# Kernel optimization log

Measured on AMD Instinct MI355X. Metric: run time of the kernel, lower is better.

The kernel has to match this reference:

```python
import jax, jax.numpy as jnp
import numpy as np

N = 1048576   # points per render chunk (16384 rays x 64 samples)
W = 64        # MLP width
IN = 32       # n_features_per_level * n_levels
LD = 36
HC = 15       # num_hidcolordim


def _linear_params(key, fan_in, fan_out):
    kw, kb = jax.random.split(key)
    bound = 1.0 / np.sqrt(fan_in)
    Wm = jax.random.uniform(kw, (fan_in, fan_out), jnp.float32, -bound, bound)
    b = jax.random.uniform(kb, (fan_out,), jnp.float32, -bound, bound)
    return Wm, b


def setup_inputs() -> dict:
    key = jax.random.key(0)
    ks = jax.random.split(key, 10)
    emb_points = jax.random.normal(ks[0], (N, IN), jnp.float32)
    enc_dir = jax.random.normal(ks[1], (N, LD + 3), jnp.float32)
    W_in, b_in = _linear_params(ks[2], IN, W)          # MLPinput
    W0, b0 = _linear_params(ks[3], W, W)               # MLPmid0 (num_hiddense=1)
    Wd, bd = _linear_params(ks[4], W, 1 + HC)          # Denseout
    Wc, bc = _linear_params(ks[5], HC + LD + 3, W)     # colorlayerin
    W1a, b1a = _linear_params(ks[6], W, W)             # MLPmid1 layer 0
    W1b, b1b = _linear_params(ks[7], W, W)             # MLPmid1 layer 1
    Wo, bo = _linear_params(ks[8], W, 3)               # colorout
    return dict(emb_points=emb_points, enc_dir=enc_dir,
                W_in=W_in, b_in=b_in, W0=W0, b0=b0, Wd=Wd, bd=bd,
                Wc=Wc, bc=bc, W1a=W1a, b1a=b1a, W1b=W1b, b1b=b1b,
                Wo=Wo, bo=bo)


def reference(emb_points, enc_dir, W_in, b_in, W0, b0, Wd, bd,
              Wc, bc, W1a, b1a, W1b, b1b, Wo, bo):
    relu = jax.nn.relu
    x = relu(emb_points @ W_in + b_in)          # [N, 64]
    x = relu(x @ W0 + b0)                       # MLPmid0
    x = x @ Wd + bd                             # [N, 16]
    dense = x[..., :1]                          # density, no activation
    h = x[..., 1:]                              # [N, 15]
    h = relu(jnp.concatenate([h, enc_dir], axis=-1) @ Wc + bc)  # [N, 64]
    h = relu(h @ W1a + b1a)                     # MLPmid1
    h = relu(h @ W1b + b1b)
    color = h @ Wo + bo                         # [N, 3]
    return jnp.concatenate([color, dense], axis=-1)  # [N, 4]
```

## Files before the change

### kernel.cpp

```cpp
#include <hip/hip_runtime.h>


#define WAVES_PER_BLOCK 8
#define BLOCK 512
#define GRID 512
#define XSTR 72
#define NFRAG 40

typedef _Float16 half8 __attribute__((ext_vector_type(8)));
typedef _Float16 half4 __attribute__((ext_vector_type(4)));
typedef _Float16 half2v __attribute__((ext_vector_type(2)));
typedef float float4v __attribute__((ext_vector_type(4)));
typedef float float4u __attribute__((ext_vector_type(4), aligned(4)));

__device__ __forceinline__ half8 wfrag(const float* W, int ld, int row0, int col, int nrow) {
  half8 r;
#pragma unroll
  for (int j = 0; j < 8; ++j) {
    int rr = row0 + j;
    float v = (rr < nrow) ? W[(size_t)rr * ld + col] : 0.f;
    r[j] = (_Float16)v;
  }
  return r;
}

__device__ half8 make_frag(int f, int q, int c,
                           const float* Win, const float* W0m, const float* Wd,
                           const float* Wc, const float* W1a, const float* W1b,
                           const float* Wo) {
  if (f < 4) return wfrag(Win, 64, 8 * q, 16 * f + c, 32);
  if (f < 12) { int t = (f - 4) >> 1, ks = (f - 4) & 1;
    return wfrag(W0m, 64, 32 * ks + 8 * q, 16 * t + c, 64); }
  if (f < 14) { int ks = f - 12;
    return wfrag(Wd, 16, 32 * ks + 8 * q, c, 64); }
  if (f < 22) { int t = (f - 14) >> 1, ks = (f - 14) & 1;
    half8 r;
#pragma unroll
    for (int j = 0; j < 8; ++j) {
      int k = 32 * ks + 8 * q + j;
      float v;
      if (k < 39) v = Wc[(size_t)(15 + k) * 64 + 16 * t + c];
      else if (k < 54) v = Wc[(size_t)(k - 39) * 64 + 16 * t + c];
      else v = 0.f;
      r[j] = (_Float16)v;
    }
    return r; }
  if (f < 30) { int t = (f - 22) >> 1, ks = (f - 22) & 1;
    return wfrag(W1a, 64, 32 * ks + 8 * q, 16 * t + c, 64); }
  if (f < 38) { int t = (f - 30) >> 1, ks = (f - 30) & 1;
    return wfrag(W1b, 64, 32 * ks + 8 * q, 16 * t + c, 64); }
  { int ks = f - 38;
    half8 r;
#pragma unroll
    for (int j = 0; j < 8; ++j) {
      float v = (c < 3) ? Wo[(size_t)(32 * ks + 8 * q + j) * 3 + c] : 0.f;
      r[j] = (_Float16)v;
    }
    return r; }
}

__global__ __launch_bounds__(BLOCK, 4) void nerf_fused(
    const float* __restrict__ emb, const float* __restrict__ enc,
    const float* __restrict__ Win, const float* __restrict__ bin,
    const float* __restrict__ W0m, const float* __restrict__ b0v,
    const float* __restrict__ Wd, const float* __restrict__ bd,
    const float* __restrict__ Wc, const float* __restrict__ bc,
    const float* __restrict__ W1a, const float* __restrict__ b1a,
    const float* __restrict__ W1b, const float* __restrict__ b1b,
    const float* __restrict__ Wo, const float* __restrict__ bo,
    float* __restrict__ out, int npts)
{
  __shared__ __align__(16) _Float16 s_w[NFRAG * 512];
  __shared__ __align__(16) float s_bias[352];
  __shared__ __align__(16) _Float16 s_X[WAVES_PER_BLOCK][32 * XSTR];

  const int tid = threadIdx.x;
  const int wib = tid >> 6;
  const int lane = tid & 63;
  const int q = lane >> 4;
  const int c = lane & 15;

  for (int i = tid; i < 352; i += BLOCK) {
    float v;
    if (i < 64) v = bin[i];
    else if (i < 128) v = b0v[i - 64];
    else if (i < 144) v = bd[i - 128];
    else if (i < 208) v = bc[i - 144];
    else if (i < 272) v = b1a[i - 208];
    else if (i < 336) v = b1b[i - 272];
    else v = (i - 336 < 3) ? bo[i - 336] : 0.f;
    s_bias[i] = v;
  }

  for (int f = wib * 5; f < wib * 5 + 5; ++f) {
    half8 r = make_frag(f, q, c, Win, W0m, Wd, Wc, W1a, W1b, Wo);
    *(half8*)&s_w[f * 512 + lane * 8] = r;
  }

  __syncthreads();

  _Float16* Xw = &s_X[wib][0];
#define OSTP(p) ((float*)(Xw + (p) * XSTR + 64))

  const int totalWaves = gridDim.x * WAVES_PER_BLOCK;
  const int waveId = blockIdx.x * WAVES_PER_BLOCK + wib;
  const int ntiles = npts >> 5;

  int tile = waveId;
  if (tile >= ntiles) return;

#define RW(f) (*(const half8*)&s_w[(f) * 512 + lane * 8])

  float4v e0[2], e1[2];
  float4u na0[2], na1[2], nb[2];
#pragma unroll
  for (int g = 0; g < 2; ++g) { na0[g] = (float4u){0,0,0,0}; na1[g] = (float4u){0,0,0,0}; nb[g] = (float4u){0,0,0,0}; }
  {
#pragma unroll
    for (int g = 0; g < 2; ++g) {
      const float* ep = emb + (size_t)(tile * 32 + 16 * g + c) * 32 + 8 * q;
      e0[g] = *(const float4v*)ep;
      e1[g] = *(const float4v*)(ep + 4);
      const float* np = enc + (size_t)(tile * 32 + 16 * g + c) * 39;
      na0[g] = *(const float4u*)(np + 8 * q);
      na1[g] = *(const float4u*)(np + 8 * q + 4);
      if (q == 0) nb[g] = *(const float4u*)(np + 32);
      else if (q == 1) { nb[g][0] = np[36]; nb[g][1] = np[37]; }
      else if (q == 2) nb[g][0] = np[38];
    }
  }

  const float4v z4 = {0.f, 0.f, 0.f, 0.f};
  float4v acc[4][2];
  half8 x[2][2];

#define READX() do { \
    _Pragma("unroll") for (int g = 0; g < 2; ++g) { \
      x[g][0] = *(const half8*)&Xw[(16 * g + c) * XSTR + 8 * q]; \
      x[g][1] = *(const half8*)&Xw[(16 * g + c) * XSTR + 32 + 8 * q]; \
    } \
  } while (0)

#define LAYER64(FB, BOFF) do { \
    _Pragma("unroll") for (int t = 0; t < 4; ++t) { \
      half8 wa = RW((FB) + 2 * t), wb = RW((FB) + 2 * t + 1); \
      _Pragma("unroll") for (int g = 0; g < 2; ++g) { \
        acc[t][g] = __builtin_amdgcn_mfma_f32_16x16x32_f16(wa, x[g][0], z4, 0, 0, 0); \
        acc[t][g] = __builtin_amdgcn_mfma_f32_16x16x32_f16(wb, x[g][1], acc[t][g], 0, 0, 0); \
      } \
    } \
    _Pragma("unroll") for (int t = 0; t < 4; ++t) { \
      float4v bb = *(const float4v*)&s_bias[(BOFF) + 16 * t + 4 * q]; \
      _Pragma("unroll") for (int g = 0; g < 2; ++g) { \
        half4 h; \
        _Pragma("unroll") for (int r = 0; r < 4; ++r) \
          h[r] = (_Float16)fmaxf(acc[t][g][r] + bb[r], 0.f); \
        *(half4*)&Xw[(16 * g + c) * XSTR + 16 * t + 4 * q] = h; \
      } \
    } \
  } while (0)

  for (; tile < ntiles; tile += totalWaves) {
    const int nt0 = tile + totalWaves;
    const int nextTile = (nt0 < ntiles) ? nt0 : tile;

    half8 bf[2];
#pragma unroll
    for (int g = 0; g < 2; ++g)
#pragma unroll
      for (int j = 0; j < 4; ++j) { bf[g][j] = (_Float16)e0[g][j]; bf[g][4 + j] = (_Float16)e1[g][j]; }
    {
#pragma unroll
      for (int g = 0; g < 2; ++g) {
        const float* ep = emb + (size_t)(nextTile * 32 + 16 * g + c) * 32 + 8 * q;
        e0[g] = *(const float4v*)ep;
        e1[g] = *(const float4v*)(ep + 4);
      }
    }
#pragma unroll
    for (int t = 0; t < 4; ++t) {
      half8 wt = RW(t);
#pragma unroll
      for (int g = 0; g < 2; ++g)
        acc[t][g] = __builtin_amdgcn_mfma_f32_16x16x32_f16(wt, bf[g], z4, 0, 0, 0);
    }
#pragma unroll
    for (int t = 0; t < 4; ++t) {
      float4v bb = *(const float4v*)&s_bias[0 + 16 * t + 4 * q];
#pragma unroll
      for (int g = 0; g < 2; ++g) {
        half4 h;
#pragma unroll
        for (int r = 0; r < 4; ++r) h[r] = (_Float16)fmaxf(acc[t][g][r] + bb[r], 0.f);
        *(half4*)&Xw[(16 * g + c) * XSTR + 16 * t + 4 * q] = h;
      }
    }

    READX();
    LAYER64(4, 64);

    READX();
    float4v a3[2];
    {
      half8 wa = RW(12), wb = RW(13);
#pragma unroll
      for (int g = 0; g < 2; ++g) {
        a3[g] = __builtin_amdgcn_mfma_f32_16x16x32_f16(wa, x[g][0], z4, 0, 0, 0);
        a3[g] = __builtin_amdgcn_mfma_f32_16x16x32_f16(wb, x[g][1], a3[g], 0, 0, 0);
      }
    }

#pragma unroll
    for (int g = 0; g < 2; ++g) {
      _Float16* Xp = &Xw[(16 * g + c) * XSTR];
      half8 ha;
#pragma unroll
      for (int j = 0; j < 4; ++j) { ha[j] = (_Float16)na0[g][j]; ha[4 + j] = (_Float16)na1[g][j]; }
      *(half8*)&Xp[8 * q] = ha;
      if (q == 0) {
        half4 hb;
#pragma unroll
        for (int r = 0; r < 4; ++r) hb[r] = (_Float16)nb[g][r];
        *(half4*)&Xp[32] = hb;
      } else if (q == 1) {
        half2v hb; hb[0] = (_Float16)nb[g][0]; hb[1] = (_Float16)nb[g][1];
        *(half2v*)&Xp[36] = hb;
      } else if (q == 2) {
        Xp[38] = (_Float16)nb[g][0];
      } else {
        half2v zz2 = {(_Float16)0.f, (_Float16)0.f};
        *(half2v*)&Xp[54] = zz2;
        half8 zz8 = {};
        *(half8*)&Xp[56] = zz8;
      }
    }
    {
#pragma unroll
      for (int g = 0; g < 2; ++g) {
        const float* np = enc + (size_t)(nextTile * 32 + 16 * g + c) * 39;
        na0[g] = *(const float4u*)(np + 8 * q);
        na1[g] = *(const float4u*)(np + 8 * q + 4);
        if (q == 0) nb[g] = *(const float4u*)(np + 32);
        else if (q == 1) { nb[g][0] = np[36]; nb[g][1] = np[37]; }
        else if (q == 2) nb[g][0] = np[38];
      }
    }

    {
      float4v bb = *(const float4v*)&s_bias[128 + 4 * q];
#pragma unroll
      for (int g = 0; g < 2; ++g)
#pragma unroll
        for (int r = 0; r < 4; ++r) {
          float v = a3[g][r] + bb[r];
          int f = 4 * q + r;
          if (f == 0) OSTP(16 * g + c)[3] = v;
          else Xw[(16 * g + c) * XSTR + 38 + f] = (_Float16)v;
        }
    }

    READX();
    LAYER64(14, 144);

    READX();
    LAYER64(22, 208);
    READX();
    LAYER64(30, 272);

    READX();
    {
      half8 wa = RW(38), wb = RW(39);
      float4v bb = *(const float4v*)&s_bias[336 + 4 * q];
#pragma unroll
      for (int g = 0; g < 2; ++g) {
        float4v a7 = __builtin_amdgcn_mfma_f32_16x16x32_f16(wa, x[g][0], z4, 0, 0, 0);
        a7 = __builtin_amdgcn_mfma_f32_16x16x32_f16(wb, x[g][1], a7, 0, 0, 0);
        if (q == 0) {
          float* op = OSTP(16 * g + c);
          op[0] = a7[0] + bb[0];
          op[1] = a7[1] + bb[1];
          op[2] = a7[2] + bb[2];
        }
      }
    }

    out[(size_t)tile * 128 + lane]      = OSTP(lane >> 2)[lane & 3];
    out[(size_t)tile * 128 + 64 + lane] = OSTP(16 + (lane >> 2))[lane & 3];
  }
#undef READX
#undef LAYER64
#undef RW
#undef OSTP
}

extern "C" void kernel_launch(void* const* d_in, const int* in_sizes, int n_in,
                              void* d_out, int out_size, void* d_ws, size_t ws_size,
                              hipStream_t stream) {
  (void)d_ws; (void)ws_size; (void)out_size;
  if (n_in < 16) return;
  const float* emb = (const float*)d_in[0];
  const float* enc = (const float*)d_in[1];
  const float* Win = (const float*)d_in[2];
  const float* bin = (const float*)d_in[3];
  const float* W0m = (const float*)d_in[4];
  const float* b0v = (const float*)d_in[5];
  const float* Wd  = (const float*)d_in[6];
  const float* bd  = (const float*)d_in[7];
  const float* Wc  = (const float*)d_in[8];
  const float* bc  = (const float*)d_in[9];
  const float* W1a = (const float*)d_in[10];
  const float* b1a = (const float*)d_in[11];
  const float* W1b = (const float*)d_in[12];
  const float* b1b = (const float*)d_in[13];
  const float* Wo  = (const float*)d_in[14];
  const float* bo  = (const float*)d_in[15];
  float* out = (float*)d_out;
  const int npts = in_sizes[0] / 32;

  nerf_fused<<<GRID, BLOCK, 0, stream>>>(emb, enc, Win, bin, W0m, b0v, Wd, bd,
                                         Wc, bc, W1a, b1a, W1b, b1b, Wo, bo,
                                         out, npts);
}
```

Before: 355.0 us.

## Keep MLP activations in registers via permuted-K weight fragments, drop LDS staging

Permutes the K ordering of the packed weight fragments so that each MFMA output fragment (4 rows per lane) can be fed straight back as the B operand of the next layer. Activations therefore stay in registers instead of being written to and read back from a per-wave LDS buffer. The biases are folded into the MFMA accumulator init, and outputs are written directly as float4 per point. This removes LDS round-trips and the per-wave LDS allocation, which may raise occupancy, but it makes the Wc concat layout and its weight packing more intricate.

```diff
diff --git a/kernel.cpp b/kernel.cpp
--- a/kernel.cpp
+++ b/kernel.cpp
@@ -4,59 +4,85 @@
 #define WAVES_PER_BLOCK 8
 #define BLOCK 512
 #define GRID 512
-#define XSTR 72
 #define NFRAG 40
 
 typedef _Float16 half8 __attribute__((ext_vector_type(8)));
 typedef _Float16 half4 __attribute__((ext_vector_type(4)));
-typedef _Float16 half2v __attribute__((ext_vector_type(2)));
 typedef float float4v __attribute__((ext_vector_type(4)));
 typedef float float4u __attribute__((ext_vector_type(4), aligned(4)));
 
-__device__ __forceinline__ half8 wfrag(const float* W, int ld, int row0, int col, int nrow) {
-  half8 r;
-#pragma unroll
-  for (int j = 0; j < 8; ++j) {
-    int rr = row0 + j;
-    float v = (rr < nrow) ? W[(size_t)rr * ld + col] : 0.f;
-    r[j] = (_Float16)v;
-  }
-  return r;
+#define CAT8(a, b) __builtin_shufflevector((a), (b), 0, 1, 2, 3, 4, 5, 6, 7)
+
+__device__ __forceinline__ int permk(int u, int q, int j) {
+  return 32 * u + 16 * (j >> 2) + 4 * q + (j & 3);
 }
 
 __device__ half8 make_frag(int f, int q, int c,
                            const float* Win, const float* W0m, const float* Wd,
                            const float* Wc, const float* W1a, const float* W1b,
                            const float* Wo) {
-  if (f < 4) return wfrag(Win, 64, 8 * q, 16 * f + c, 32);
-  if (f < 12) { int t = (f - 4) >> 1, ks = (f - 4) & 1;
-    return wfrag(W0m, 64, 32 * ks + 8 * q, 16 * t + c, 64); }
-  if (f < 14) { int ks = f - 12;
-    return wfrag(Wd, 16, 32 * ks + 8 * q, c, 64); }
-  if (f < 22) { int t = (f - 14) >> 1, ks = (f - 14) & 1;
-    half8 r;
-#pragma unroll
-    for (int j = 0; j < 8; ++j) {
-      int k = 32 * ks + 8 * q + j;
-      float v;
-      if (k < 39) v = Wc[(size_t)(15 + k) * 64 + 16 * t + c];
-      else if (k < 54) v = Wc[(size_t)(k - 39) * 64 + 16 * t + c];
-      else v = 0.f;
-      r[j] = (_Float16)v;
-    }
-    return r; }
-  if (f < 30) { int t = (f - 22) >> 1, ks = (f - 22) & 1;
-    return wfrag(W1a, 64, 32 * ks + 8 * q, 16 * t + c, 64); }
-  if (f < 38) { int t = (f - 30) >> 1, ks = (f - 30) & 1;
-    return wfrag(W1b, 64, 32 * ks + 8 * q, 16 * t + c, 64); }
-  { int ks = f - 38;
-    half8 r;
-#pragma unroll
-    for (int j = 0; j < 8; ++j) {
-      float v = (c < 3) ? Wo[(size_t)(32 * ks + 8 * q + j) * 3 + c] : 0.f;
-      r[j] = (_Float16)v;
-    }
-    return r; }
+  half8 r;
+  if (f < 4) {
+#pragma unroll
+    for (int j = 0; j < 8; ++j)
+      r[j] = (_Float16)Win[(size_t)(8 * q + j) * 64 + 16 * f + c];
+    return r;
+  }
+  if (f < 12) {
+    int mb = (f - 4) >> 1, u = (f - 4) & 1;
+#pragma unroll
+    for (int j = 0; j < 8; ++j)
+      r[j] = (_Float16)W0m[(size_t)permk(u, q, j) * 64 + 16 * mb + c];
+    return r;
+  }
+  if (f < 14) {
+    int u = f - 12;
+#pragma unroll
+    for (int j = 0; j < 8; ++j)
+      r[j] = (_Float16)Wd[(size_t)permk(u, q, j) * 16 + c];
+    return r;
+  }
+  if (f < 22) {
+    int mb = (f - 14) >> 1, u = (f - 14) & 1;
+    if (u == 0) {
+#pragma unroll
+      for (int i = 0; i < 4; ++i) {
+        int hs = 4 * q + i;
+        r[i] = (hs == 0) ? (_Float16)0.f
+                         : (_Float16)Wc[(size_t)(hs - 1) * 64 + 16 * mb + c];
+        int e = 32 + 4 * q + i;
+        r[4 + i] = (e < 39) ? (_Float16)Wc[(size_t)(15 + e) * 64 + 16 * mb + c]
+                            : (_Float16)0.f;
+      }
+    } else {
+#pragma unroll
+      for (int j = 0; j < 8; ++j)
+        r[j] = (_Float16)Wc[(size_t)(15 + 8 * q + j) * 64 + 16 * mb + c];
+    }
+    return r;
+  }
+  if (f < 30) {
+    int mb = (f - 22) >> 1, u = (f - 22) & 1;
+#pragma unroll
+    for (int j = 0; j < 8; ++j)
+      r[j] = (_Float16)W1a[(size_t)permk(u, q, j) * 64 + 16 * mb + c];
+    return r;
+  }
+  if (f < 38) {
+    int mb = (f - 30) >> 1, u = (f - 30) & 1;
+#pragma unroll
+    for (int j = 0; j < 8; ++j)
+      r[j] = (_Float16)W1b[(size_t)permk(u, q, j) * 64 + 16 * mb + c];
+    return r;
+  }
+  {
+    int u = f - 38;
+#pragma unroll
+    for (int j = 0; j < 8; ++j)
+      r[j] = (c < 3) ? (_Float16)Wo[(size_t)permk(u, q, j) * 3 + c]
+                     : (_Float16)0.f;
+    return r;
+  }
 }
 
 __global__ __launch_bounds__(BLOCK, 4) void nerf_fused(
@@ -72,7 +98,6 @@
 {
   __shared__ __align__(16) _Float16 s_w[NFRAG * 512];
   __shared__ __align__(16) float s_bias[352];
-  __shared__ __align__(16) _Float16 s_X[WAVES_PER_BLOCK][32 * XSTR];
 
   const int tid = threadIdx.x;
   const int wib = tid >> 6;
@@ -99,9 +124,6 @@
 
   __syncthreads();
 
-  _Float16* Xw = &s_X[wib][0];
-#define OSTP(p) ((float*)(Xw + (p) * XSTR + 64))
-
   const int totalWaves = gridDim.x * WAVES_PER_BLOCK;
   const int waveId = blockIdx.x * WAVES_PER_BLOCK + wib;
   const int ntiles = npts >> 5;
@@ -109,66 +131,60 @@
   int tile = waveId;
   if (tile >= ntiles) return;
 
-#define RW(f) (*(const half8*)&s_w[(f) * 512 + lane * 8])
+#define RW8(f) (*(const half8*)&s_w[(f) * 512 + lane * 8])
+#define MM32(w, b, cc) __builtin_amdgcn_mfma_f32_16x16x32_f16((w), (b), (cc), 0, 0, 0)
 
   float4v e0[2], e1[2];
-  float4u na0[2], na1[2], nb[2];
-#pragma unroll
-  for (int g = 0; g < 2; ++g) { na0[g] = (float4u){0,0,0,0}; na1[g] = (float4u){0,0,0,0}; nb[g] = (float4u){0,0,0,0}; }
-  {
-#pragma unroll
-    for (int g = 0; g < 2; ++g) {
-      const float* ep = emb + (size_t)(tile * 32 + 16 * g + c) * 32 + 8 * q;
-      e0[g] = *(const float4v*)ep;
-      e1[g] = *(const float4v*)(ep + 4);
-      const float* np = enc + (size_t)(tile * 32 + 16 * g + c) * 39;
-      na0[g] = *(const float4u*)(np + 8 * q);
-      na1[g] = *(const float4u*)(np + 8 * q + 4);
-      if (q == 0) nb[g] = *(const float4u*)(np + 32);
-      else if (q == 1) { nb[g][0] = np[36]; nb[g][1] = np[37]; }
-      else if (q == 2) nb[g][0] = np[38];
-    }
-  }
-
-  const float4v z4 = {0.f, 0.f, 0.f, 0.f};
-  float4v acc[4][2];
-  half8 x[2][2];
-
-#define READX() do { \
+  float4u na0[2], na1[2], e2p[2];
+#pragma unroll
+  for (int g = 0; g < 2; ++g) e2p[g] = (float4u){0.f, 0.f, 0.f, 0.f};
+#pragma unroll
+  for (int g = 0; g < 2; ++g) {
+    const float* ep = emb + (size_t)(tile * 32 + 16 * g + c) * 32 + 8 * q;
+    e0[g] = *(const float4v*)ep;
+    e1[g] = *(const float4v*)(ep + 4);
+    const float* np = enc + (size_t)(tile * 32 + 16 * g + c) * 39;
+    na0[g] = *(const float4u*)(np + 8 * q);
+    na1[g] = *(const float4u*)(np + 8 * q + 4);
+    if (q == 0) e2p[g] = *(const float4u*)(np + 32);
+    else if (q == 1) { e2p[g][0] = np[36]; e2p[g][1] = np[37]; e2p[g][2] = np[38]; }
+  }
+
+  float4v a_[4][2];
+  half4 x[4][2];
+
+#define LAYER64(FB, BOFF) do { \
+    half8 b1_[2], b2_[2]; \
     _Pragma("unroll") for (int g = 0; g < 2; ++g) { \
-      x[g][0] = *(const half8*)&Xw[(16 * g + c) * XSTR + 8 * q]; \
-      x[g][1] = *(const half8*)&Xw[(16 * g + c) * XSTR + 32 + 8 * q]; \
+      b1_[g] = CAT8(x[0][g], x[1][g]); \
+      b2_[g] = CAT8(x[2][g], x[3][g]); \
     } \
-  } while (0)
-
-#define LAYER64(FB, BOFF) do { \
-    _Pragma("unroll") for (int t = 0; t < 4; ++t) { \
-      half8 wa = RW((FB) + 2 * t), wb = RW((FB) + 2 * t + 1); \
+    _Pragma("unroll") for (int mb = 0; mb < 4; ++mb) { \
+      float4v bb = *(const float4v*)&s_bias[(BOFF) + 16 * mb + 4 * q]; \
+      half8 w0 = RW8((FB) + 2 * mb), w1 = RW8((FB) + 2 * mb + 1); \
       _Pragma("unroll") for (int g = 0; g < 2; ++g) { \
-        acc[t][g] = __builtin_amdgcn_mfma_f32_16x16x32_f16(wa, x[g][0], z4, 0, 0, 0); \
-        acc[t][g] = __builtin_amdgcn_mfma_f32_16x16x32_f16(wb, x[g][1], acc[t][g], 0, 0, 0); \
+        float4v a = MM32(w0, b1_[g], bb); \
+        a_[mb][g] = MM32(w1, b2_[g], a); \
       } \
     } \
-    _Pragma("unroll") for (int t = 0; t < 4; ++t) { \
-      float4v bb = *(const float4v*)&s_bias[(BOFF) + 16 * t + 4 * q]; \
+    _Pragma("unroll") for (int mb = 0; mb < 4; ++mb) \
       _Pragma("unroll") for (int g = 0; g < 2; ++g) { \
         half4 h; \
         _Pragma("unroll") for (int r = 0; r < 4; ++r) \
-          h[r] = (_Float16)fmaxf(acc[t][g][r] + bb[r], 0.f); \
-        *(half4*)&Xw[(16 * g + c) * XSTR + 16 * t + 4 * q] = h; \
+          h[r] = (_Float16)fmaxf(a_[mb][g][r], 0.f); \
+        x[mb][g] = h; \
       } \
-    } \
   } while (0)
 
   for (; tile < ntiles; tile += totalWaves) {
     const int nt0 = tile + totalWaves;
     const int nextTile = (nt0 < ntiles) ? nt0 : tile;
 
-    half8 bf[2];
+    half8 bfe[2];
 #pragma unroll
     for (int g = 0; g < 2; ++g)
 #pragma unroll
-      for (int j = 0; j < 4; ++j) { bf[g][j] = (_Float16)e0[g][j]; bf[g][4 + j] = (_Float16)e1[g][j]; }
+      for (int j = 0; j < 4; ++j) { bfe[g][j] = (_Float16)e0[g][j]; bfe[g][4 + j] = (_Float16)e1[g][j]; }
     {
 #pragma unroll
       for (int g = 0; g < 2; ++g) {
@@ -178,61 +194,49 @@
       }
     }
 #pragma unroll
-    for (int t = 0; t < 4; ++t) {
-      half8 wt = RW(t);
-#pragma unroll
-      for (int g = 0; g < 2; ++g)
-        acc[t][g] = __builtin_amdgcn_mfma_f32_16x16x32_f16(wt, bf[g], z4, 0, 0, 0);
-    }
-#pragma unroll
-    for (int t = 0; t < 4; ++t) {
-      float4v bb = *(const float4v*)&s_bias[0 + 16 * t + 4 * q];
+    for (int mb = 0; mb < 4; ++mb) {
+      float4v bb = *(const float4v*)&s_bias[0 + 16 * mb + 4 * q];
+      half8 w = RW8(mb);
+#pragma unroll
+      for (int g = 0; g < 2; ++g) a_[mb][g] = MM32(w, bfe[g], bb);
+    }
+#pragma unroll
+    for (int mb = 0; mb < 4; ++mb)
 #pragma unroll
       for (int g = 0; g < 2; ++g) {
         half4 h;
 #pragma unroll
-        for (int r = 0; r < 4; ++r) h[r] = (_Float16)fmaxf(acc[t][g][r] + bb[r], 0.f);
-        *(half4*)&Xw[(16 * g + c) * XSTR + 16 * t + 4 * q] = h;
-      }
-    }
-
-    READX();
+        for (int r = 0; r < 4; ++r) h[r] = (_Float16)fmaxf(a_[mb][g][r], 0.f);
+        x[mb][g] = h;
+      }
+
     LAYER64(4, 64);
 
-    READX();
-    float4v a3[2];
+    float dense_[2];
+    half4 xh[2];
     {
-      half8 wa = RW(12), wb = RW(13);
-#pragma unroll
-      for (int g = 0; g < 2; ++g) {
-        a3[g] = __builtin_amdgcn_mfma_f32_16x16x32_f16(wa, x[g][0], z4, 0, 0, 0);
-        a3[g] = __builtin_amdgcn_mfma_f32_16x16x32_f16(wb, x[g][1], a3[g], 0, 0, 0);
-      }
-    }
-
+      half8 w0 = RW8(12), w1 = RW8(13);
+      float4v bb = *(const float4v*)&s_bias[128 + 4 * q];
+#pragma unroll
+      for (int g = 0; g < 2; ++g) {
+        half8 b1_ = CAT8(x[0][g], x[1][g]);
+        half8 b2_ = CAT8(x[2][g], x[3][g]);
+        float4v a = MM32(w0, b1_, bb);
+        a = MM32(w1, b2_, a);
+        dense_[g] = a[0];
+#pragma unroll
+        for (int r = 0; r < 4; ++r) xh[g][r] = (_Float16)a[r];
+      }
+    }
+
+    half8 xe32[2];
+    half4 xe16[2];
 #pragma unroll
     for (int g = 0; g < 2; ++g) {
-      _Float16* Xp = &Xw[(16 * g + c) * XSTR];
-      half8 ha;
-#pragma unroll
-      for (int j = 0; j < 4; ++j) { ha[j] = (_Float16)na0[g][j]; ha[4 + j] = (_Float16)na1[g][j]; }
-      *(half8*)&Xp[8 * q] = ha;
-      if (q == 0) {
-        half4 hb;
-#pragma unroll
-        for (int r = 0; r < 4; ++r) hb[r] = (_Float16)nb[g][r];
-        *(half4*)&Xp[32] = hb;
-      } else if (q == 1) {
-        half2v hb; hb[0] = (_Float16)nb[g][0]; hb[1] = (_Float16)nb[g][1];
-        *(half2v*)&Xp[36] = hb;
-      } else if (q == 2) {
-        Xp[38] = (_Float16)nb[g][0];
-      } else {
-        half2v zz2 = {(_Float16)0.f, (_Float16)0.f};
-        *(half2v*)&Xp[54] = zz2;
-        half8 zz8 = {};
-        *(half8*)&Xp[56] = zz8;
-      }
+#pragma unroll
+      for (int j = 0; j < 4; ++j) { xe32[g][j] = (_Float16)na0[g][j]; xe32[g][4 + j] = (_Float16)na1[g][j]; }
+#pragma unroll
+      for (int i = 0; i < 4; ++i) xe16[g][i] = (_Float16)e2p[g][i];
     }
     {
 #pragma unroll
@@ -240,57 +244,55 @@
         const float* np = enc + (size_t)(nextTile * 32 + 16 * g + c) * 39;
         na0[g] = *(const float4u*)(np + 8 * q);
         na1[g] = *(const float4u*)(np + 8 * q + 4);
-        if (q == 0) nb[g] = *(const float4u*)(np + 32);
-        else if (q == 1) { nb[g][0] = np[36]; nb[g][1] = np[37]; }
-        else if (q == 2) nb[g][0] = np[38];
-      }
-    }
+        if (q == 0) e2p[g] = *(const float4u*)(np + 32);
+        else if (q == 1) { e2p[g][0] = np[36]; e2p[g][1] = np[37]; e2p[g][2] = np[38]; }
+      }
+    }
+
+#pragma unroll
+    for (int mb = 0; mb < 4; ++mb) {
+      float4v bb = *(const float4v*)&s_bias[144 + 16 * mb + 4 * q];
+      half8 wA = RW8(14 + 2 * mb), wE = RW8(15 + 2 * mb);
+#pragma unroll
+      for (int g = 0; g < 2; ++g) {
+        half8 bh = CAT8(xh[g], xe16[g]);
+        float4v a = MM32(wA, bh, bb);
+        a_[mb][g] = MM32(wE, xe32[g], a);
+      }
+    }
+#pragma unroll
+    for (int mb = 0; mb < 4; ++mb)
+#pragma unroll
+      for (int g = 0; g < 2; ++g) {
+        half4 h;
+#pragma unroll
+        for (int r = 0; r < 4; ++r) h[r] = (_Float16)fmaxf(a_[mb][g][r], 0.f);
+        x[mb][g] = h;
+      }
+
+    LAYER64(22, 208);
+    LAYER64(30, 272);
 
     {
-      float4v bb = *(const float4v*)&s_bias[128 + 4 * q];
-#pragma unroll
-      for (int g = 0; g < 2; ++g)
-#pragma unroll
-        for (int r = 0; r < 4; ++r) {
-          float v = a3[g][r] + bb[r];
-          int f = 4 * q + r;
-          if (f == 0) OSTP(16 * g + c)[3] = v;
-          else Xw[(16 * g + c) * XSTR + 38 + f] = (_Float16)v;
+      half8 w0 = RW8(38), w1 = RW8(39);
+      float4v bb = *(const float4v*)&s_bias[336 + 4 * q];
+#pragma unroll
+      for (int g = 0; g < 2; ++g) {
+        half8 b1_ = CAT8(x[0][g], x[1][g]);
+        half8 b2_ = CAT8(x[2][g], x[3][g]);
+        float4v a = MM32(w0, b1_, bb);
+        a = MM32(w1, b2_, a);
+        if (q == 0) {
+          float4v o;
+          o[0] = a[0]; o[1] = a[1]; o[2] = a[2]; o[3] = dense_[g];
+          *(float4v*)(out + (size_t)(tile * 32 + 16 * g + c) * 4) = o;
         }
-    }
-
-    READX();
-    LAYER64(14, 144);
-
-    READX();
-    LAYER64(22, 208);
-    READX();
-    LAYER64(30, 272);
-
-    READX();
-    {
-      half8 wa = RW(38), wb = RW(39);
-      float4v bb = *(const float4v*)&s_bias[336 + 4 * q];
-#pragma unroll
-      for (int g = 0; g < 2; ++g) {
-        float4v a7 = __builtin_amdgcn_mfma_f32_16x16x32_f16(wa, x[g][0], z4, 0, 0, 0);
-        a7 = __builtin_amdgcn_mfma_f32_16x16x32_f16(wb, x[g][1], a7, 0, 0, 0);
-        if (q == 0) {
-          float* op = OSTP(16 * g + c);
-          op[0] = a7[0] + bb[0];
-          op[1] = a7[1] + bb[1];
-          op[2] = a7[2] + bb[2];
-        }
-      }
-    }
-
-    out[(size_t)tile * 128 + lane]      = OSTP(lane >> 2)[lane & 3];
-    out[(size_t)tile * 128 + 64 + lane] = OSTP(16 + (lane >> 2))[lane & 3];
-  }
-#undef READX
+      }
+    }
+  }
 #undef LAYER64
-#undef RW
-#undef OSTP
+#undef RW8
+#undef MM32
 }
 
 extern "C" void kernel_launch(void* const* d_in, const int* in_sizes, int n_in,
```

Result: slower. 751.0 us (+111.5%).
